# Kernel optimization log

Hardware: AMD Instinct MI355X
Metric: run time of the kernel (lower is better)

Reference implementation:

```python
import jax, jax.numpy as jnp
import numpy as np

NUM_CLASSES = 80
NUM_ANCHORS = 5
IGNORE_THRESH = 0.5
COORD_SCALE = 1.0
NOOBJ_SCALE = 1.0
OBJ_SCALE = 5.0
CLASS_SCALE = 1.0


def iou_xywh(a, b):
    # a: (N,4), b: (K,4) in center format (cx,cy,w,h) -> (N,K) IoU
    tl = jnp.maximum(a[:, None, :2] - a[:, None, 2:] * 0.5, b[None, :, :2] - b[None, :, 2:] * 0.5)
    br = jnp.minimum(a[:, None, :2] + a[:, None, 2:] * 0.5, b[None, :, :2] + b[None, :, 2:] * 0.5)
    area_a = a[:, 2] * a[:, 3]
    area_b = b[:, 2] * b[:, 3]
    en = jnp.all(tl < br, axis=2).astype(a.dtype)
    area_i = jnp.prod(br - tl, axis=2) * en
    return area_i / (area_a[:, None] + area_b[None, :] - area_i + 1e-12)


def make_pred_boxes(outputs, anchors):
    B, C, H, W = outputs.shape
    A = NUM_ANCHORS
    o = outputs.reshape(B, A, 5 + NUM_CLASSES, H, W).transpose(0, 1, 3, 4, 2)  # (B,A,H,W,ch)
    xs = jnp.arange(W, dtype=o.dtype)
    ys = jnp.arange(H, dtype=o.dtype)
    bx = jax.nn.sigmoid(o[..., 0]) + xs[None, None, None, :]
    by = jax.nn.sigmoid(o[..., 1]) + ys[None, None, :, None]
    bw = jnp.exp(o[..., 2]) * anchors[:, 0][None, :, None, None]
    bh = jnp.exp(o[..., 3]) * anchors[:, 1][None, :, None, None]
    bx = jnp.clip(bx, 0, W); bw = jnp.clip(bw, 0, W)
    by = jnp.clip(by, 0, H); bh = jnp.clip(bh, 0, H)
    pred = jnp.stack([bx, by, bw, bh], axis=-1).transpose(0, 2, 3, 1, 4).reshape(B, H * W, A, 4)
    xg = jnp.broadcast_to(xs[None, None, :], (A, H, W))
    yg = jnp.broadcast_to(ys[None, :, None], (A, H, W))
    wa = jnp.broadcast_to(anchors[:, 0][:, None, None], (A, H, W))
    ha = jnp.broadcast_to(anchors[:, 1][:, None, None], (A, H, W))
    anchors_x1y1 = jnp.stack([xg, yg, wa, ha]).transpose(2, 3, 1, 0).reshape(H * W, A, 4)
    return pred, anchors_x1y1


def build_targets(pred_boxes, anchors_x1y1, targets, H, W):
    HW, A = anchors_x1y1.shape[:2]
    anchors_xcyc = anchors_x1y1.at[..., :2].add(0.5)
    M = targets.shape[1]
    scale = jnp.array([W, H, W, H], dtype=pred_boxes.dtype)

    def one(pred, tgt):
        num_obj = jnp.sum(jnp.sum(tgt, axis=1) > 0)
        valid = jnp.arange(M) < num_obj
        gt_boxes = tgt[:, 1:] * scale  # (M,4) in grid units
        gt_cls = tgt[:, 0]
        ious = iou_xywh(pred.reshape(-1, 4), gt_boxes).reshape(HW, A, M)
        ious = jnp.where(valid[None, None, :], ious, -1.0)
        max_iou = jnp.max(ious, axis=-1)  # (HW, A)
        apply_ign = jnp.any(max_iou > IGNORE_THRESH)
        iou_m0 = jnp.where(apply_ign & (max_iou >= IGNORE_THRESH), 0.0, 1.0)
        overlaps = iou_xywh(anchors_xcyc.reshape(-1, 4), gt_boxes).reshape(HW, A, M)
        overlaps = jnp.where(valid[None, None, :], overlaps, -1.0)
        ov_t = overlaps.transpose(2, 0, 1)  # (M, HW, A)

        z = jnp.zeros((HW, A), pred.dtype)
        carry0 = (z, iou_m0, jnp.zeros((HW, A, 4), pred.dtype), z, z, z, z)

        def step(carry, xs):
            iou_t, iou_m, box_t, box_m, box_s, cls_t, cls_m = carry
            gt_box, gcls, v, ov = xs
            cell = (jnp.floor(gt_box[1]) * W + jnp.floor(gt_box[0])).astype(jnp.int32)
            a_idx = jnp.argmax(ov[cell])
            anc = anchors_x1y1[cell, a_idx]
            delta = jnp.stack([gt_box[0] - anc[0], gt_box[1] - anc[1],
                               gt_box[2] / anc[2], gt_box[3] / anc[3]])
            pb = pred[cell, a_idx]
            s = 2.0 - (pb[2] / W) * (pb[3] / H)

            def upd(arr, val):
                return jnp.where(v, arr.at[cell, a_idx].set(val), arr)

            carry = (upd(iou_t, max_iou[cell, a_idx]), upd(iou_m, 2.0),
                     upd(box_t, delta), upd(box_m, 1.0), upd(box_s, s),
                     upd(cls_t, gcls), upd(cls_m, 1.0))
            return carry, None

        (iou_t, iou_m, box_t, box_m, box_s, cls_t, cls_m), _ = jax.lax.scan(
            step, carry0, (gt_boxes, gt_cls, valid, ov_t))
        iou_m = jnp.where(num_obj > 0, iou_m, jnp.zeros_like(iou_m))
        return iou_t, iou_m, box_t, box_m, box_s, cls_t, cls_m

    return jax.vmap(one)(pred_boxes, targets)


def yolov2_loss(outputs, targets, anchors):
    B, C, H, W = outputs.shape
    A, nc = NUM_ANCHORS, NUM_CLASSES
    det = jax.lax.stop_gradient(outputs)     # torch: build_targets(outputs.detach(), ...)
    tgt = jax.lax.stop_gradient(targets)     # ground truth: no grad
    anc = jax.lax.stop_gradient(anchors)
    pred_boxes, anchors_x1y1 = make_pred_boxes(det, anc)
    iou_t, iou_m, box_t, box_m, box_s, cls_t, cls_m = build_targets(pred_boxes, anchors_x1y1, tgt, H, W)

    o = outputs.reshape(B, A, 5 + nc, H, W).transpose(0, 3, 4, 1, 2).reshape(-1, 5 + nc)
    deltas = jnp.concatenate([jax.nn.sigmoid(o[:, :2]), jnp.exp(o[:, 2:4])], axis=1)
    conf = jax.nn.sigmoid(o[:, 4])
    logits = o[:, 5:]

    iou_t = iou_t.reshape(-1); iou_m = iou_m.reshape(-1)
    box_t = box_t.reshape(-1, 4); box_m = box_m.reshape(-1); box_s = box_s.reshape(-1)
    cls_t = cls_t.reshape(-1).astype(jnp.int32); cls_m = cls_m.reshape(-1)

    wdiff = (deltas - box_t) * (box_m * box_s)[:, None]
    box_loss = COORD_SCALE * jnp.sum(wdiff ** 2) / 2.0 / B

    csq = (conf - iou_t) ** 2
    iou_loss = (NOOBJ_SCALE * jnp.sum((iou_m == 1.0) * csq)
                + OBJ_SCALE * jnp.sum((iou_m == 2.0) * csq)) / 2.0 / B

    logp = jax.nn.log_softmax(logits, axis=-1)
    ce = -jnp.take_along_axis(logp, cls_t[:, None], axis=1)[:, 0]
    class_loss = CLASS_SCALE * jnp.sum(cls_m * ce) / B
    return box_loss + iou_loss + class_loss


def setup_inputs() -> dict:
    key = jax.random.key(0)
    k0, k1, k2, k3, k4, k5 = jax.random.split(key, 6)
    B, H, W, M = 64, 52, 52, 50
    C = NUM_ANCHORS * (5 + NUM_CLASSES)
    outputs = jax.random.normal(k0, (B, C, H, W), jnp.float32) * 0.5
    anchors = jax.random.uniform(k1, (NUM_ANCHORS, 2), jnp.float32, 1.0, 8.0)
    num_obj = jax.random.randint(k2, (B,), 1, M + 1)
    cls = jax.random.randint(k3, (B, M, 1), 0, NUM_CLASSES).astype(jnp.float32)
    cxy = jax.random.uniform(k4, (B, M, 2), jnp.float32, 0.02, 0.98)
    wh = jax.random.uniform(k5, (B, M, 2), jnp.float32, 0.05, 0.5)
    targets = jnp.concatenate([cls, cxy, wh], axis=2)
    valid = (jnp.arange(M)[None, :] < num_obj[:, None])[..., None].astype(jnp.float32)
    targets = targets * valid  # valid objects are a nonzero prefix, rest all-zero
    return {"outputs": outputs, "targets": targets, "anchors": anchors}


def reference(outputs, targets, anchors):
    return yolov2_loss(outputs, targets, anchors)
```

## Files before the change

### kernel.cpp

```cpp
#include <hip/hip_runtime.h>
#include <math.h>

#define NUM_CLASSES 80
#define A_ 5
#define B_ 64
#define H_ 52
#define W_ 52
#define M_ 50
#define C_ (A_ * (5 + NUM_CLASSES))
#define HW_ (H_ * W_)
#define ROWS_PER_B (A_ * HW_)
#define BPB 53

struct WS {
    float gsum[4];
    float s_all[B_];
    float s_lt[B_];
    int   flag[B_];
    int   num_obj[B_];
    int   rec_row[B_ * M_];
    int   rec_cls[B_ * M_];
    float rec_s[B_ * M_];
    float rec_d[B_ * M_ * 4];
};

__device__ __forceinline__ float frcp(float x) { return __builtin_amdgcn_rcpf(x); }

__device__ __forceinline__ float iou_box(float ax1, float ay1, float ax2, float ay2, float aa,
                                         float bx1, float by1, float bx2, float by2, float ba) {
    float tlx = fmaxf(ax1, bx1), tly = fmaxf(ay1, by1);
    float brx = fminf(ax2, bx2), bry = fminf(ay2, by2);
    float ix = fmaxf(brx - tlx, 0.0f), iy = fmaxf(bry - tly, 0.0f);
    float inter = ix * iy;
    return inter * frcp(aa + ba - inter + 1e-12f);
}

__global__ void k_assign(const float* __restrict__ out, const float* __restrict__ tgt,
                         const float* __restrict__ anc, WS* __restrict__ ws) {
    int b = blockIdx.x;
    int m = threadIdx.x;
    __shared__ float sgx[M_], sgy[M_], sgw[M_], sgh[M_], scls[M_];
    __shared__ int svalid[M_], skey[M_];

    if (m < M_) {
        const float* t = tgt + ((long)b * M_ + m) * 5;
        float c0 = t[0], c1 = t[1], c2 = t[2], c3 = t[3], c4 = t[4];
        svalid[m] = (c0 + c1 + c2 + c3 + c4) > 0.0f;
        scls[m] = c0;
        sgx[m] = c1 * (float)W_;
        sgy[m] = c2 * (float)H_;
        sgw[m] = c3 * (float)W_;
        sgh[m] = c4 * (float)H_;
    }
    if (threadIdx.x == 0) { ws->s_all[b] = 0.0f; ws->s_lt[b] = 0.0f; ws->flag[b] = 0; }
    if (b == 0 && threadIdx.x < 4) ws->gsum[threadIdx.x] = 0.0f;
    __syncthreads();

    if (m < M_) {
        int key = -1;
        if (svalid[m]) {
            float gx = sgx[m], gy = sgy[m], gw = sgw[m], gh = sgh[m];
            int cx = (int)floorf(gx), cy = (int)floorf(gy);
            float bx1 = gx - gw * 0.5f, by1 = gy - gh * 0.5f;
            float bx2 = gx + gw * 0.5f, by2 = gy + gh * 0.5f, ba = gw * gh;
            float best = -1e30f;
            int bi = 0;
            float axc = (float)cx + 0.5f, ayc = (float)cy + 0.5f;
            for (int a = 0; a < A_; a++) {
                float wa = anc[2 * a], ha = anc[2 * a + 1];
                float o = iou_box(axc - wa * 0.5f, ayc - ha * 0.5f,
                                  axc + wa * 0.5f, ayc + ha * 0.5f, wa * ha,
                                  bx1, by1, bx2, by2, ba);
                if (o > best) { best = o; bi = a; }
            }
            key = (cy * W_ + cx) * A_ + bi;
            float wa = anc[2 * bi], ha = anc[2 * bi + 1];
            long base = ((long)b * C_ + bi * 85) * HW_ + cy * W_ + cx;
            float pw = fminf(__expf(out[base + 2 * HW_]) * wa, (float)W_);
            float ph = fminf(__expf(out[base + 3 * HW_]) * ha, (float)H_);
            int idx = b * M_ + m;
            ws->rec_cls[idx] = (int)scls[m];
            ws->rec_s[idx]   = 2.0f - (pw * (1.0f / (float)W_)) * (ph * (1.0f / (float)H_));
            ws->rec_d[idx * 4 + 0] = gx - (float)cx;
            ws->rec_d[idx * 4 + 1] = gy - (float)cy;
            ws->rec_d[idx * 4 + 2] = gw * frcp(wa);
            ws->rec_d[idx * 4 + 3] = gh * frcp(ha);
        }
        skey[m] = key;
    }
    __syncthreads();
    if (m < M_) {
        int key = skey[m];
        int winner = (key >= 0);
        if (winner) {
            for (int mm = m + 1; mm < M_; mm++)
                if (skey[mm] == key) { winner = 0; break; }
        }
        ws->rec_row[b * M_ + m] = winner ? key : -1;
    }
    if (threadIdx.x == 0) {
        int cnt = 0;
        for (int i = 0; i < M_; i++) cnt += svalid[i];
        ws->num_obj[b] = cnt;
    }
}

__global__ __launch_bounds__(256) void k_main(const float* __restrict__ out,
                                              const float* __restrict__ tgt,
                                              const float* __restrict__ anc,
                                              WS* __restrict__ ws) {
    int b = blockIdx.x / BPB;
    int blk = blockIdx.x - b * BPB;
    int local = blk * 256 + threadIdx.x;
    int tid = threadIdx.x;

    __shared__ float sx1[M_], sy1[M_], sx2[M_], sy2[M_], sab[M_];
    __shared__ int srow[M_], scls[M_];
    __shared__ float sds[M_], sd0[M_], sd1[M_], sd2[M_], sd3[M_];
    __shared__ int snum;
    __shared__ float wred[4][5];
    __shared__ int wflag[4];

    int myvalid = 0;
    if (tid < M_) {
        const float* t = tgt + ((long)b * M_ + tid) * 5;
        float c0 = t[0], c1 = t[1], c2 = t[2], c3 = t[3], c4 = t[4];
        myvalid = (c0 + c1 + c2 + c3 + c4) > 0.0f;
        float gx = c1 * (float)W_, gy = c2 * (float)H_;
        float gw = c3 * (float)W_, gh = c4 * (float)H_;
        sx1[tid] = gx - gw * 0.5f; sy1[tid] = gy - gh * 0.5f;
        sx2[tid] = gx + gw * 0.5f; sy2[tid] = gy + gh * 0.5f;
        sab[tid] = gw * gh;
    } else if (tid >= 64 && tid < 64 + M_) {
        int m = tid - 64, idx = b * M_ + m;
        srow[m] = ws->rec_row[idx];
        scls[m] = ws->rec_cls[idx];
        sds[m]  = ws->rec_s[idx];
        sd0[m] = ws->rec_d[idx * 4 + 0];
        sd1[m] = ws->rec_d[idx * 4 + 1];
        sd2[m] = ws->rec_d[idx * 4 + 2];
        sd3[m] = ws->rec_d[idx * 4 + 3];
    }
    if (tid < 64) {
        unsigned long long bv = __ballot(myvalid);
        if (tid == 0) snum = (int)__popcll(bv);
    }
    __syncthreads();
    int n = snum;

    float t_obj = 0.0f, t_box = 0.0f, t_cls = 0.0f, t_all = 0.0f, t_lt = 0.0f;
    int myflag = 0;

    if (local < ROWS_PER_B) {
        int a = local / HW_;
        int rem = local - a * HW_;
        int h = rem / W_;
        int w = rem - h * W_;
        const float* p = out + ((long)b * C_ + a * 85) * HW_ + rem;
        float o0 = p[0], o1 = p[HW_], o2 = p[2 * HW_], o3 = p[3 * HW_], o4 = p[4 * HW_];
        float sgx = frcp(1.0f + __expf(-o0));
        float sgy = frcp(1.0f + __expf(-o1));
        float ew = __expf(o2), eh = __expf(o3);
        float wa = anc[2 * a], ha = anc[2 * a + 1];
        float px = fminf(fmaxf(sgx + (float)w, 0.0f), (float)W_);
        float py = fminf(fmaxf(sgy + (float)h, 0.0f), (float)H_);
        float pw = fminf(ew * wa, (float)W_);
        float ph = fminf(eh * ha, (float)H_);
        float conf = frcp(1.0f + __expf(-o4));

        float px1 = px - pw * 0.5f, py1 = py - ph * 0.5f;
        float px2 = px + pw * 0.5f, py2 = py + ph * 0.5f, pa = pw * ph;

        float max_iou = -1.0f;
        for (int m = 0; m < n; m++) {
            float tlx = fmaxf(px1, sx1[m]), tly = fmaxf(py1, sy1[m]);
            float brx = fminf(px2, sx2[m]), bry = fminf(py2, sy2[m]);
            float ix = fmaxf(brx - tlx, 0.0f), iy = fmaxf(bry - tly, 0.0f);
            float inter = ix * iy;
            float iou = inter * frcp(pa + sab[m] - inter + 1e-12f);
            max_iou = fmaxf(max_iou, iou);
        }
        myflag = (max_iou > 0.5f);

        int keyrow = (h * W_ + w) * A_ + a;
        int rec = -1;
        for (int m = 0; m < n; m++)
            if (srow[m] == keyrow) rec = m;

        if (rec >= 0) {
            float d = conf - max_iou;
            t_obj = d * d;
            float sc = sds[rec];
            float e0 = (sgx - sd0[rec]) * sc, e1 = (sgy - sd1[rec]) * sc;
            float e2 = (ew - sd2[rec]) * sc,  e3 = (eh - sd3[rec]) * sc;
            t_box = e0 * e0 + e1 * e1 + e2 * e2 + e3 * e3;
            const float* lp = p + 5 * HW_;
            float mx = -1e30f;
            for (int c = 0; c < NUM_CLASSES; c++) mx = fmaxf(mx, lp[c * HW_]);
            float s = 0.0f;
            for (int c = 0; c < NUM_CLASSES; c++) s += __expf(lp[c * HW_] - mx);
            float lc = lp[scls[rec] * HW_];
            t_cls = __logf(s) + mx - lc;
        } else {
            t_all = conf * conf;
            t_lt = (max_iou < 0.5f) ? t_all : 0.0f;
        }
    }

    for (int off = 32; off > 0; off >>= 1) {
        t_obj += __shfl_down(t_obj, off);
        t_box += __shfl_down(t_box, off);
        t_cls += __shfl_down(t_cls, off);
        t_all += __shfl_down(t_all, off);
        t_lt  += __shfl_down(t_lt, off);
    }
    unsigned long long bal = __ballot(myflag);
    int wid = tid >> 6;
    if ((tid & 63) == 0) {
        wred[wid][0] = t_obj; wred[wid][1] = t_box; wred[wid][2] = t_cls;
        wred[wid][3] = t_all; wred[wid][4] = t_lt;
        wflag[wid] = (bal != 0ull);
    }
    __syncthreads();
    if (tid == 0) {
        float obj = 0, box = 0, cls = 0, all = 0, lt = 0;
        int fl = 0;
        for (int i = 0; i < 4; i++) {
            obj += wred[i][0]; box += wred[i][1]; cls += wred[i][2];
            all += wred[i][3]; lt  += wred[i][4]; fl |= wflag[i];
        }
        if (obj != 0.0f) atomicAdd(&ws->gsum[0], obj);
        if (box != 0.0f) atomicAdd(&ws->gsum[1], box);
        if (cls != 0.0f) atomicAdd(&ws->gsum[2], cls);
        atomicAdd(&ws->s_all[b], all);
        atomicAdd(&ws->s_lt[b], lt);
        if (fl) atomicOr(&ws->flag[b], 1);
    }
}

__global__ void k_final(WS* __restrict__ ws, float* __restrict__ outp) {
    int b = threadIdx.x;
    float v = 0.0f;
    if (b < B_ && ws->num_obj[b] > 0)
        v = ws->flag[b] ? ws->s_lt[b] : ws->s_all[b];
    for (int off = 32; off > 0; off >>= 1) v += __shfl_down(v, off);
    if (b == 0) {
        float obj = ws->gsum[0], box = ws->gsum[1], cls = ws->gsum[2];
        float inv2B = 1.0f / (2.0f * (float)B_);
        float loss = box * inv2B + (v + 5.0f * obj) * inv2B + cls * (1.0f / (float)B_);
        outp[0] = loss;
    }
}

extern "C" void kernel_launch(void* const* d_in, const int* in_sizes, int n_in,
                              void* d_out, int out_size, void* d_ws, size_t ws_size,
                              hipStream_t stream) {
    const float* outputs = (const float*)d_in[0];
    const float* targets = (const float*)d_in[1];
    const float* anchors = (const float*)d_in[2];
    WS* ws = (WS*)d_ws;
    float* o = (float*)d_out;

    hipLaunchKernelGGL(k_assign, dim3(B_), dim3(64), 0, stream, outputs, targets, anchors, ws);
    hipLaunchKernelGGL(k_main, dim3(B_ * BPB), dim3(256), 0, stream, outputs, targets, anchors, ws);
    hipLaunchKernelGGL(k_final, dim3(1), dim3(64), 0, stream, ws, o);
}
```

Measured before the change: 389.1 us.

## Move per-record cross-entropy into a wave-parallel kernel and drop atomics

The 80-class softmax cross-entropy moves out of k_main into a new kernel, k_ce. There it runs with one 64-lane wave per target record instead of a single divergent thread looping serially over strided loads. k_assign now precomputes ground-truth boxes and areas in the workspace, so k_main reads them with uniform (scalar-friendly) loads instead of staging them in shared memory. k_main also folds the record-match search into the IoU loop, and writes per-block partial sums that k_final reduces, replacing global atomics and the zero-init. The cost is an extra kernel launch and more workspace traffic.

```diff
diff --git a/kernel.cpp b/kernel.cpp
--- a/kernel.cpp
+++ b/kernel.cpp
@@ -7,21 +7,22 @@
 #define H_ 52
 #define W_ 52
 #define M_ 50
-#define C_ (A_ * (5 + NUM_CLASSES))
-#define HW_ (H_ * W_)
-#define ROWS_PER_B (A_ * HW_)
+#define C_ 425
+#define HW_ 2704
+#define ROWS_PER_B 13520
 #define BPB 53
+#define NREC (B_ * M_)
 
 struct WS {
-    float gsum[4];
-    float s_all[B_];
-    float s_lt[B_];
-    int   flag[B_];
     int   num_obj[B_];
-    int   rec_row[B_ * M_];
-    int   rec_cls[B_ * M_];
-    float rec_s[B_ * M_];
-    float rec_d[B_ * M_ * 4];
+    int   rec_row[NREC];
+    int   rec_cls[NREC];
+    float rec_s[NREC];
+    float rec_d[NREC * 4];
+    float rec_ce[NREC];
+    float gt_box[NREC * 4];
+    float gt_area[NREC];
+    float blk[B_ * BPB][5];
 };
 
 __device__ __forceinline__ float frcp(float x) { return __builtin_amdgcn_rcpf(x); }
@@ -47,13 +48,16 @@
         float c0 = t[0], c1 = t[1], c2 = t[2], c3 = t[3], c4 = t[4];
         svalid[m] = (c0 + c1 + c2 + c3 + c4) > 0.0f;
         scls[m] = c0;
-        sgx[m] = c1 * (float)W_;
-        sgy[m] = c2 * (float)H_;
-        sgw[m] = c3 * (float)W_;
-        sgh[m] = c4 * (float)H_;
-    }
-    if (threadIdx.x == 0) { ws->s_all[b] = 0.0f; ws->s_lt[b] = 0.0f; ws->flag[b] = 0; }
-    if (b == 0 && threadIdx.x < 4) ws->gsum[threadIdx.x] = 0.0f;
+        float gx = c1 * (float)W_, gy = c2 * (float)H_;
+        float gw = c3 * (float)W_, gh = c4 * (float)H_;
+        sgx[m] = gx; sgy[m] = gy; sgw[m] = gw; sgh[m] = gh;
+        int idx = b * M_ + m;
+        ws->gt_box[idx * 4 + 0] = gx - gw * 0.5f;
+        ws->gt_box[idx * 4 + 1] = gy - gh * 0.5f;
+        ws->gt_box[idx * 4 + 2] = gx + gw * 0.5f;
+        ws->gt_box[idx * 4 + 3] = gy + gh * 0.5f;
+        ws->gt_area[idx] = gw * gh;
+    }
     __syncthreads();
 
     if (m < M_) {
@@ -105,50 +109,55 @@
     }
 }
 
+__global__ __launch_bounds__(256) void k_ce(const float* __restrict__ out,
+                                            const int* __restrict__ rrow,
+                                            const int* __restrict__ rcls,
+                                            float* __restrict__ rce) {
+    int r = (int)((blockIdx.x * 256 + threadIdx.x) >> 6);
+    int lane = threadIdx.x & 63;
+    if (r >= NREC) return;
+    int key = rrow[r];
+    if (key < 0) {
+        if (lane == 0) rce[r] = 0.0f;
+        return;
+    }
+    int b = r / M_;
+    int cellhw = key / A_;
+    int a = key - cellhw * A_;
+    const float* lp = out + ((long)b * C_ + a * 85 + 5) * HW_ + cellhw;
+    float x0 = lp[(long)lane * HW_];
+    float x1 = (lane < NUM_CLASSES - 64) ? lp[(long)(lane + 64) * HW_] : -1e30f;
+    float mx = fmaxf(x0, x1);
+    for (int off = 32; off > 0; off >>= 1) mx = fmaxf(mx, __shfl_down(mx, off));
+    mx = __shfl(mx, 0);
+    float s = __expf(x0 - mx) + ((lane < NUM_CLASSES - 64) ? __expf(x1 - mx) : 0.0f);
+    for (int off = 32; off > 0; off >>= 1) s += __shfl_down(s, off);
+    if (lane == 0) {
+        float lc = lp[(long)rcls[r] * HW_];
+        rce[r] = __logf(s) + mx - lc;
+    }
+}
+
 __global__ __launch_bounds__(256) void k_main(const float* __restrict__ out,
-                                              const float* __restrict__ tgt,
                                               const float* __restrict__ anc,
-                                              WS* __restrict__ ws) {
+                                              const float4* __restrict__ gtbox,
+                                              const float* __restrict__ gtarea,
+                                              const int* __restrict__ rrow,
+                                              const float* __restrict__ rs,
+                                              const float4* __restrict__ rd,
+                                              const int* __restrict__ nobj,
+                                              float* __restrict__ blk) {
     int b = blockIdx.x / BPB;
-    int blk = blockIdx.x - b * BPB;
-    int local = blk * 256 + threadIdx.x;
+    int blki = blockIdx.x - b * BPB;
+    int local = blki * 256 + threadIdx.x;
     int tid = threadIdx.x;
-
-    __shared__ float sx1[M_], sy1[M_], sx2[M_], sy2[M_], sab[M_];
-    __shared__ int srow[M_], scls[M_];
-    __shared__ float sds[M_], sd0[M_], sd1[M_], sd2[M_], sd3[M_];
-    __shared__ int snum;
+    int bm0 = b * M_;
+    int n = nobj[b];
+
     __shared__ float wred[4][5];
     __shared__ int wflag[4];
 
-    int myvalid = 0;
-    if (tid < M_) {
-        const float* t = tgt + ((long)b * M_ + tid) * 5;
-        float c0 = t[0], c1 = t[1], c2 = t[2], c3 = t[3], c4 = t[4];
-        myvalid = (c0 + c1 + c2 + c3 + c4) > 0.0f;
-        float gx = c1 * (float)W_, gy = c2 * (float)H_;
-        float gw = c3 * (float)W_, gh = c4 * (float)H_;
-        sx1[tid] = gx - gw * 0.5f; sy1[tid] = gy - gh * 0.5f;
-        sx2[tid] = gx + gw * 0.5f; sy2[tid] = gy + gh * 0.5f;
-        sab[tid] = gw * gh;
-    } else if (tid >= 64 && tid < 64 + M_) {
-        int m = tid - 64, idx = b * M_ + m;
-        srow[m] = ws->rec_row[idx];
-        scls[m] = ws->rec_cls[idx];
-        sds[m]  = ws->rec_s[idx];
-        sd0[m] = ws->rec_d[idx * 4 + 0];
-        sd1[m] = ws->rec_d[idx * 4 + 1];
-        sd2[m] = ws->rec_d[idx * 4 + 2];
-        sd3[m] = ws->rec_d[idx * 4 + 3];
-    }
-    if (tid < 64) {
-        unsigned long long bv = __ballot(myvalid);
-        if (tid == 0) snum = (int)__popcll(bv);
-    }
-    __syncthreads();
-    int n = snum;
-
-    float t_obj = 0.0f, t_box = 0.0f, t_cls = 0.0f, t_all = 0.0f, t_lt = 0.0f;
+    float t_obj = 0.0f, t_box = 0.0f, t_all = 0.0f, t_lt = 0.0f;
     int myflag = 0;
 
     if (local < ROWS_PER_B) {
@@ -171,36 +180,35 @@
         float px1 = px - pw * 0.5f, py1 = py - ph * 0.5f;
         float px2 = px + pw * 0.5f, py2 = py + ph * 0.5f, pa = pw * ph;
 
+        int keyrow = (h * W_ + w) * A_ + a;
+        int rec = -1;
         float max_iou = -1.0f;
+        const float4* gb = gtbox + bm0;
+        const float*  ga = gtarea + bm0;
+        const int*    rr = rrow + bm0;
         for (int m = 0; m < n; m++) {
-            float tlx = fmaxf(px1, sx1[m]), tly = fmaxf(py1, sy1[m]);
-            float brx = fminf(px2, sx2[m]), bry = fminf(py2, sy2[m]);
+            float4 g = gb[m];
+            float garea = ga[m];
+            int key = rr[m];
+            float tlx = fmaxf(px1, g.x), tly = fmaxf(py1, g.y);
+            float brx = fminf(px2, g.z), bry = fminf(py2, g.w);
             float ix = fmaxf(brx - tlx, 0.0f), iy = fmaxf(bry - tly, 0.0f);
             float inter = ix * iy;
-            float iou = inter * frcp(pa + sab[m] - inter + 1e-12f);
+            float iou = inter * frcp(pa + garea - inter + 1e-12f);
             max_iou = fmaxf(max_iou, iou);
+            rec = (key == keyrow) ? m : rec;
         }
         myflag = (max_iou > 0.5f);
 
-        int keyrow = (h * W_ + w) * A_ + a;
-        int rec = -1;
-        for (int m = 0; m < n; m++)
-            if (srow[m] == keyrow) rec = m;
-
         if (rec >= 0) {
+            int idx = bm0 + rec;
             float d = conf - max_iou;
             t_obj = d * d;
-            float sc = sds[rec];
-            float e0 = (sgx - sd0[rec]) * sc, e1 = (sgy - sd1[rec]) * sc;
-            float e2 = (ew - sd2[rec]) * sc,  e3 = (eh - sd3[rec]) * sc;
+            float sc = rs[idx];
+            float4 dd = rd[idx];
+            float e0 = (sgx - dd.x) * sc, e1 = (sgy - dd.y) * sc;
+            float e2 = (ew - dd.z) * sc,  e3 = (eh - dd.w) * sc;
             t_box = e0 * e0 + e1 * e1 + e2 * e2 + e3 * e3;
-            const float* lp = p + 5 * HW_;
-            float mx = -1e30f;
-            for (int c = 0; c < NUM_CLASSES; c++) mx = fmaxf(mx, lp[c * HW_]);
-            float s = 0.0f;
-            for (int c = 0; c < NUM_CLASSES; c++) s += __expf(lp[c * HW_] - mx);
-            float lc = lp[scls[rec] * HW_];
-            t_cls = __logf(s) + mx - lc;
         } else {
             t_all = conf * conf;
             t_lt = (max_iou < 0.5f) ? t_all : 0.0f;
@@ -210,45 +218,50 @@
     for (int off = 32; off > 0; off >>= 1) {
         t_obj += __shfl_down(t_obj, off);
         t_box += __shfl_down(t_box, off);
-        t_cls += __shfl_down(t_cls, off);
         t_all += __shfl_down(t_all, off);
         t_lt  += __shfl_down(t_lt, off);
     }
     unsigned long long bal = __ballot(myflag);
     int wid = tid >> 6;
     if ((tid & 63) == 0) {
-        wred[wid][0] = t_obj; wred[wid][1] = t_box; wred[wid][2] = t_cls;
-        wred[wid][3] = t_all; wred[wid][4] = t_lt;
+        wred[wid][0] = t_obj; wred[wid][1] = t_box;
+        wred[wid][2] = t_all; wred[wid][3] = t_lt;
         wflag[wid] = (bal != 0ull);
     }
     __syncthreads();
     if (tid == 0) {
-        float obj = 0, box = 0, cls = 0, all = 0, lt = 0;
+        float obj = 0, box = 0, all = 0, lt = 0;
         int fl = 0;
         for (int i = 0; i < 4; i++) {
-            obj += wred[i][0]; box += wred[i][1]; cls += wred[i][2];
-            all += wred[i][3]; lt  += wred[i][4]; fl |= wflag[i];
-        }
-        if (obj != 0.0f) atomicAdd(&ws->gsum[0], obj);
-        if (box != 0.0f) atomicAdd(&ws->gsum[1], box);
-        if (cls != 0.0f) atomicAdd(&ws->gsum[2], cls);
-        atomicAdd(&ws->s_all[b], all);
-        atomicAdd(&ws->s_lt[b], lt);
-        if (fl) atomicOr(&ws->flag[b], 1);
-    }
-}
-
-__global__ void k_final(WS* __restrict__ ws, float* __restrict__ outp) {
+            obj += wred[i][0]; box += wred[i][1];
+            all += wred[i][2]; lt  += wred[i][3]; fl |= wflag[i];
+        }
+        float* o = blk + (long)blockIdx.x * 5;
+        o[0] = obj; o[1] = box; o[2] = all; o[3] = lt; o[4] = fl ? 1.0f : 0.0f;
+    }
+}
+
+__global__ void k_final(const WS* __restrict__ ws, float* __restrict__ outp) {
     int b = threadIdx.x;
-    float v = 0.0f;
-    if (b < B_ && ws->num_obj[b] > 0)
-        v = ws->flag[b] ? ws->s_lt[b] : ws->s_all[b];
-    for (int off = 32; off > 0; off >>= 1) v += __shfl_down(v, off);
+    float obj = 0, box = 0, all = 0, lt = 0;
+    int fl = 0;
+    for (int k = 0; k < BPB; k++) {
+        const float* p = ws->blk[b * BPB + k];
+        obj += p[0]; box += p[1]; all += p[2]; lt += p[3];
+        fl |= (p[4] != 0.0f);
+    }
+    float v = (ws->num_obj[b] > 0) ? (fl ? lt : all) : 0.0f;
+    float cls = 0;
+    for (int r = b; r < NREC; r += 64) cls += ws->rec_ce[r];
+    for (int off = 32; off > 0; off >>= 1) {
+        obj += __shfl_down(obj, off);
+        box += __shfl_down(box, off);
+        v   += __shfl_down(v, off);
+        cls += __shfl_down(cls, off);
+    }
     if (b == 0) {
-        float obj = ws->gsum[0], box = ws->gsum[1], cls = ws->gsum[2];
         float inv2B = 1.0f / (2.0f * (float)B_);
-        float loss = box * inv2B + (v + 5.0f * obj) * inv2B + cls * (1.0f / (float)B_);
-        outp[0] = loss;
+        outp[0] = box * inv2B + (v + 5.0f * obj) * inv2B + cls * (1.0f / (float)B_);
     }
 }
 
@@ -262,6 +275,12 @@
     float* o = (float*)d_out;
 
     hipLaunchKernelGGL(k_assign, dim3(B_), dim3(64), 0, stream, outputs, targets, anchors, ws);
-    hipLaunchKernelGGL(k_main, dim3(B_ * BPB), dim3(256), 0, stream, outputs, targets, anchors, ws);
+    hipLaunchKernelGGL(k_main, dim3(B_ * BPB), dim3(256), 0, stream,
+                       outputs, anchors,
+                       (const float4*)ws->gt_box, ws->gt_area,
+                       ws->rec_row, ws->rec_s, (const float4*)ws->rec_d,
+                       ws->num_obj, (float*)ws->blk);
+    hipLaunchKernelGGL(k_ce, dim3((NREC * 64 + 255) / 256), dim3(256), 0, stream,
+                       outputs, ws->rec_row, ws->rec_cls, ws->rec_ce);
     hipLaunchKernelGGL(k_final, dim3(1), dim3(64), 0, stream, ws, o);
 }
```

Result: faster. 371.5 us (-4.5%).
